# Kernel optimization log

Hardware: AMD Instinct MI355X
Metric: run time of the kernel (lower is better)

## Reference

```python
import jax, jax.numpy as jnp
from jax import lax
import numpy as np

P = 9          # patch_size (hardcoded in CUTSEncoder)
HALF = P // 2  # 4
EPS = 1e-5     # BatchNorm eps (torch default)
SLOPE = 0.01   # LeakyReLU negative slope (torch default)


def _conv(x, w, b):
    # 3x3 'same' conv, NCHW / OIHW
    y = lax.conv_general_dilated(x, w, (1, 1), 'SAME',
                                 dimension_numbers=('NCHW', 'OIHW', 'NCHW'))
    return y + b[None, :, None, None]


def _bn(x, gamma, beta):
    # training-mode BatchNorm2d: batch statistics over (N,H,W)
    m = jnp.mean(x, axis=(0, 2, 3), keepdims=True)
    v = jnp.var(x, axis=(0, 2, 3), keepdims=True)
    return gamma[None, :, None, None] * (x - m) * lax.rsqrt(v + EPS) + beta[None, :, None, None]


def _block(x, w, b, g, be):
    return jax.nn.leaky_relu(_bn(_conv(x, w, b), g, be), SLOPE)


def setup_inputs() -> dict:
    key = jax.random.key(0)
    ks = jax.random.split(key, 16)
    B, C, H, W = 8, 3, 256, 256
    K = 32                 # num_kernels
    L = K * 8              # latent_dim = 256
    S = 32                 # sampled_patches_per_image

    x = jax.random.normal(ks[0], (B, C, H, W), jnp.float32)
    anchors_hw = jax.random.randint(ks[1], (B, S, 2), HALF, H - HALF, jnp.int32)
    positives_hw = jax.random.randint(ks[2], (B, S, 2), HALF, H - HALF, jnp.int32)

    def w_(k, shape):
        return jax.random.normal(k, shape, jnp.float32) * 0.05

    params = {
        'w1': w_(ks[3], (K, C, 3, 3)),       'b1': jnp.zeros((K,), jnp.float32),
        'g1': jnp.ones((K,), jnp.float32),   'be1': jnp.zeros((K,), jnp.float32),
        'w2': w_(ks[4], (2 * K, K, 3, 3)),   'b2': jnp.zeros((2 * K,), jnp.float32),
        'g2': jnp.ones((2 * K,), jnp.float32), 'be2': jnp.zeros((2 * K,), jnp.float32),
        'w3': w_(ks[5], (4 * K, 2 * K, 3, 3)), 'b3': jnp.zeros((4 * K,), jnp.float32),
        'g3': jnp.ones((4 * K,), jnp.float32), 'be3': jnp.zeros((4 * K,), jnp.float32),
        'w4': w_(ks[6], (8 * K, 4 * K, 3, 3)), 'b4': jnp.zeros((8 * K,), jnp.float32),
        'g4': jnp.ones((8 * K,), jnp.float32), 'be4': jnp.zeros((8 * K,), jnp.float32),
        'rw': w_(ks[7], (S * C * P * P, S * L)),  # recon Linear [out,in]
        'rb': jnp.zeros((S * C * P * P,), jnp.float32),
    }
    return dict(x=x, anchors_hw=anchors_hw, positives_hw=positives_hw, **params)


def reference(x, anchors_hw, positives_hw,
              w1, b1, g1, be1, w2, b2, g2, be2,
              w3, b3, g3, be3, w4, b4, g4, be4, rw, rb):
    B, C, H, W = x.shape
    # 4-stage conv+BN+LeakyReLU backbone -> z: [B, L, H, W]
    z = _block(x, w1, b1, g1, be1)
    z = _block(z, w2, b2, g2, be2)
    z = _block(z, w3, b3, g3, be3)
    z = _block(z, w4, b4, g4, be4)

    # batched 9x9 patch extraction around anchors: [B, S, C, P, P]
    def patch(img, hw):  # img: [C,H,W], hw: [2]
        return lax.dynamic_slice(img, (0, hw[0] - HALF, hw[1] - HALF), (C, P, P))
    x_anchors = jax.vmap(lambda img, hws: jax.vmap(lambda hw: patch(img, hw))(hws))(x, anchors_hw)

    # batched pointwise latent gathers: [B, S, L]
    def gather_z(zb, hws):  # zb: [L,H,W]
        return zb[:, hws[:, 0], hws[:, 1]].T  # [S, L]
    z_anchors = jax.vmap(gather_z)(z, anchors_hw)
    z_positives = jax.vmap(gather_z)(z, positives_hw)

    x_anchors_flat = x_anchors.reshape(B, -1)
    x_recon = z_anchors.reshape(B, -1) @ rw.T + rb
    return (z, x_anchors_flat, x_recon, z_anchors, z_positives)
```

## Files before the change

### kernel.cpp

```cpp
#include <hip/hip_runtime.h>
#include <hip/hip_bf16.h>

#define HW 65536
constexpr int IMG_W = 256;

typedef __attribute__((ext_vector_type(8))) short short8;
typedef __attribute__((ext_vector_type(4))) float f32x4;

__device__ __forceinline__ float bf2f(unsigned short u) {
    return __uint_as_float(((unsigned)u) << 16);
}
__device__ __forceinline__ unsigned short f2bf(float f) {
    __hip_bfloat16 h = __float2bfloat16(f);
    return *reinterpret_cast<unsigned short*>(&h);
}

__global__ __launch_bounds__(256) void conv1_direct(
    const float* __restrict__ x, const float* __restrict__ wt,
    const float* __restrict__ bias, unsigned short* __restrict__ outraw)
{
    constexpr int CIN = 3, COUT = 32, OCB = 16;
    const int tile = blockIdx.x;
    const int ty0 = (tile >> 3) << 5;
    const int tx0 = (tile & 7) << 5;
    const int oc0 = blockIdx.y * OCB;
    const int b = blockIdx.z;

    __shared__ alignas(16) float s_in[CIN][34][36];
    __shared__ alignas(16) float s_w[CIN][9][OCB];

    const int tid = threadIdx.x;
    const int lx = tid & 31;
    const int ly = tid >> 5;

    float acc[4][OCB];
    #pragma unroll
    for (int j = 0; j < 4; ++j)
        #pragma unroll
        for (int oc = 0; oc < OCB; ++oc) acc[j][oc] = 0.f;

    for (int idx = tid; idx < CIN * 34 * 34; idx += 256) {
        int ic  = idx / (34 * 34);
        int rem = idx - ic * (34 * 34);
        int r   = rem / 34;
        int cc  = rem - r * 34;
        int gy = ty0 - 1 + r, gx = tx0 - 1 + cc;
        float v = 0.f;
        if ((unsigned)gy < 256u && (unsigned)gx < 256u)
            v = x[((size_t)(b * CIN + ic)) * HW + (size_t)gy * IMG_W + gx];
        s_in[ic][r][cc] = v;
    }
    for (int idx = tid; idx < CIN * 9 * OCB; idx += 256) {
        int oc  = idx & (OCB - 1);
        int t2  = idx >> 4;
        int tap = t2 % 9;
        int ic  = t2 / 9;
        s_w[ic][tap][oc] = wt[((size_t)(oc0 + oc) * CIN + ic) * 9 + tap];
    }
    __syncthreads();

    for (int ic = 0; ic < CIN; ++ic) {
        #pragma unroll
        for (int tap = 0; tap < 9; ++tap) {
            const int dy = tap / 3, dx = tap % 3;
            float wr[OCB];
            #pragma unroll
            for (int q = 0; q < OCB / 4; ++q)
                *(float4*)&wr[q * 4] = *(const float4*)&s_w[ic][tap][q * 4];
            #pragma unroll
            for (int j = 0; j < 4; ++j) {
                float iv = s_in[ic][ly + 8 * j + dy][lx + dx];
                #pragma unroll
                for (int oc = 0; oc < OCB; ++oc) acc[j][oc] += iv * wr[oc];
            }
        }
    }

    #pragma unroll
    for (int j = 0; j < 4; ++j) {
        const size_t p = ((size_t)b << 16) + (size_t)((ty0 + ly + 8 * j) << 8) + tx0 + lx;
        short8 v0, v1;
        #pragma unroll
        for (int k = 0; k < 8; ++k) {
            v0[k] = (short)f2bf(acc[j][k] + bias[oc0 + k]);
            v1[k] = (short)f2bf(acc[j][8 + k] + bias[oc0 + 8 + k]);
        }
        *(short8*)&outraw[p * COUT + oc0]     = v0;
        *(short8*)&outraw[p * COUT + oc0 + 8] = v1;
    }
}

__global__ void repack2(const float* __restrict__ w, unsigned short* __restrict__ wp,
                        int COUT, int CIN)
{
    int i = blockIdx.x * 256 + threadIdx.x;
    int K9 = 9 * CIN;
    if (i >= COUT * K9) return;
    int oc = i / K9, k = i - oc * K9;
    int tap = k / CIN, ic = k - tap * CIN;
    wp[(size_t)(k >> 3) * COUT * 8 + oc * 8 + (k & 7)] =
        f2bf(w[((size_t)(oc * CIN + ic)) * 9 + tap]);
}

template<int CIN, int COUT, int WM, int WN>
__global__ __launch_bounds__(256, 3) void conv_mfma2(
    const unsigned short* __restrict__ in, const float2* __restrict__ coef,
    const unsigned short* __restrict__ wp, const float* __restrict__ bias,
    unsigned short* __restrict__ outraw, float2* __restrict__ partial)
{
    constexpr int CINP = CIN + 8;
    constexpr int ROWS = WM * 4;
    constexpr int TILES = (256 / ROWS) * 16;
    constexpr int NOC = COUT / (WN * 64);
    constexpr int NCHUNK = TILES * 8;
    constexpr int ICB = CIN / 32;
    constexpr int NOCT = CIN / 8;

    __shared__ alignas(16) short s_in[(ROWS + 2) * 18 * CINP];
    __shared__ float2 s_coef[CIN];
    __shared__ float2 s_stat[4][64];

    const int bx = blockIdx.x;
    const int tile = bx / NOC;
    const int oc0 = (bx - tile * NOC) * (WN * 64);
    const int b = blockIdx.z;
    const int ty0 = (tile >> 4) * ROWS;
    const int tx0 = (tile & 15) * 16;
    const int tid = threadIdx.x;

    if (tid < CIN) s_coef[tid] = coef[tid];
    __syncthreads();

    const size_t bbase = (size_t)b << 16;
    for (int idx = tid; idx < (ROWS + 2) * 18 * NOCT; idx += 256) {
        int ic8 = idx % NOCT;
        int rc  = idx / NOCT;
        int c = rc % 18, r = rc / 18;
        int gy = ty0 - 1 + r, gx = tx0 - 1 + c;
        short8 v = (short8)0;
        if ((unsigned)gy < 256u && (unsigned)gx < 256u) {
            short8 rawv = *(const short8*)&in[(bbase + (size_t)(gy << 8) + gx) * CIN + ic8 * 8];
            #pragma unroll
            for (int j = 0; j < 8; ++j) {
                float2 ab = s_coef[ic8 * 8 + j];
                float xv = ab.x * bf2f((unsigned short)rawv[j]) + ab.y;
                xv = xv > 0.f ? xv : 0.01f * xv;
                v[j] = (short)f2bf(xv);
            }
        }
        *(short8*)&s_in[(r * 18 + c) * CINP + ic8 * 8] = v;
    }
    __syncthreads();

    const int lane = tid & 63;
    const int wv = tid >> 6;
    const int wm = wv / WN, wn = wv % WN;
    const int ln = lane & 15;
    const int grp = lane >> 4;

    f32x4 acc[4][4] = {};

    const unsigned short* wpb = wp + ((size_t)grp * COUT + oc0 + wn * 64 + ln) * 8;

    for (int tap = 0; tap < 9; ++tap) {
        const int dy = tap / 3, dx = tap - dy * 3;
        const int arow = (wm * 4 + dy) * 18 + ln + dx;
        const int kc0 = tap * (CIN / 8);
        #pragma unroll
        for (int icb = 0; icb < ICB; ++icb) {
            short8 bfr[4];
            #pragma unroll
            for (int g = 0; g < 4; ++g)
                bfr[g] = *(const short8*)&wpb[((size_t)(kc0 + icb * 4) * COUT + g * 16) * 8];
            #pragma unroll
            for (int f = 0; f < 4; ++f) {
                short8 av = *(const short8*)&s_in[(arow + f * 18) * CINP + icb * 32 + grp * 8];
                #pragma unroll
                for (int g = 0; g < 4; ++g)
                    acc[f][g] = __builtin_amdgcn_mfma_f32_16x16x32_bf16(av, bfr[g], acc[f][g], 0, 0, 0);
            }
        }
    }

    #pragma unroll
    for (int g = 0; g < 4; ++g) {
        const int oc = oc0 + wn * 64 + g * 16 + ln;
        const float bv = bias[oc];
        float s = 0.f, q = 0.f;
        #pragma unroll
        for (int f = 0; f < 4; ++f) {
            const int rr = ty0 + wm * 4 + f;
            const size_t rowbase = (bbase + (size_t)(rr << 8) + tx0 + grp * 4) * COUT + oc;
            #pragma unroll
            for (int reg = 0; reg < 4; ++reg) {
                float v = acc[f][g][reg] + bv;
                outraw[rowbase + (size_t)reg * COUT] = f2bf(v);
                s += v; q += v * v;
            }
        }
        s += __shfl_down(s, 32); q += __shfl_down(q, 32);
        s += __shfl_down(s, 16); q += __shfl_down(q, 16);
        if (grp == 0) s_stat[wv][g * 16 + ln] = make_float2(s, q);
    }
    __syncthreads();
    if (tid < WN * 64) {
        const int wn2 = tid >> 6;
        const int ol = tid & 63;
        float sx = 0.f, sq = 0.f;
        #pragma unroll
        for (int m = 0; m < WM; ++m) {
            float2 p = s_stat[m * WN + wn2][ol];
            sx += p.x; sq += p.y;
        }
        const int chunk = b * TILES + tile;
        partial[(size_t)(oc0 + wn2 * 64 + ol) * NCHUNK + chunk] = make_float2(sx, sq);
    }
}

template<int C>
__global__ __launch_bounds__(256) void bn_stats_nhwc(const unsigned short* __restrict__ raw,
                                                     float2* __restrict__ partial)
{
    constexpr int CPT = C / 8;
    constexpr int PPI = 256 / CPT;
    const int t = threadIdx.x;
    const int co = t % CPT, pg = t / CPT;
    const int p0 = blockIdx.x * 2048;
    float s[8], ss[8];
    #pragma unroll
    for (int j = 0; j < 8; ++j) { s[j] = 0.f; ss[j] = 0.f; }
    for (int p = p0 + pg; p < p0 + 2048; p += PPI) {
        short8 v = *(const short8*)&raw[(size_t)p * C + co * 8];
        #pragma unroll
        for (int j = 0; j < 8; ++j) {
            float xv = bf2f((unsigned short)v[j]);
            s[j] += xv; ss[j] += xv * xv;
        }
    }
    __shared__ float rs[256][8], rss[256][8];
    #pragma unroll
    for (int j = 0; j < 8; ++j) { rs[t][j] = s[j]; rss[t][j] = ss[j]; }
    __syncthreads();
    for (int off = PPI / 2; off > 0; off >>= 1) {
        if (pg < off) {
            #pragma unroll
            for (int j = 0; j < 8; ++j) {
                rs[t][j]  += rs[t + off * CPT][j];
                rss[t][j] += rss[t + off * CPT][j];
            }
        }
        __syncthreads();
    }
    if (pg == 0) {
        #pragma unroll
        for (int j = 0; j < 8; ++j)
            partial[(size_t)(co * 8 + j) * 256 + blockIdx.x] = make_float2(rs[t][j], rss[t][j]);
    }
}

__global__ void bn_finalize_kernel(const float2* __restrict__ partial,
                                   const float* __restrict__ gamma,
                                   const float* __restrict__ beta,
                                   float2* __restrict__ coef, int C, int nchunk)
{
    int c = threadIdx.x;
    if (c >= C) return;
    float s = 0.f, ss = 0.f;
    for (int i = 0; i < nchunk; ++i) {
        float2 p = partial[(size_t)c * nchunk + i];
        s += p.x; ss += p.y;
    }
    const float N = 524288.f;
    float m = s / N;
    float v = ss / N - m * m;
    float rsq = rsqrtf(v + 1e-5f);
    float a = gamma[c] * rsq;
    coef[c] = make_float2(a, beta[c] - m * a);
}

template<int NCHUNK>
__global__ __launch_bounds__(256) void bn_finalize2(const float2* __restrict__ partial,
                                                    const float* __restrict__ gamma,
                                                    const float* __restrict__ beta,
                                                    float2* __restrict__ coef)
{
    const int c = blockIdx.x, t = threadIdx.x;
    float s = 0.f, q = 0.f;
    for (int i = t; i < NCHUNK; i += 256) {
        float2 p = partial[(size_t)c * NCHUNK + i];
        s += p.x; q += p.y;
    }
    __shared__ float rs[256], rq[256];
    rs[t] = s; rq[t] = q;
    __syncthreads();
    for (int off = 128; off; off >>= 1) {
        if (t < off) { rs[t] += rs[t + off]; rq[t] += rq[t + off]; }
        __syncthreads();
    }
    if (t == 0) {
        const float N = 524288.f;
        float m = rs[0] / N;
        float v = rq[0] / N - m * m;
        float a = gamma[c] * rsqrtf(v + 1e-5f);
        coef[c] = make_float2(a, beta[c] - m * a);
    }
}

__global__ __launch_bounds__(256) void apply_t(const unsigned short* __restrict__ raw,
                                               const float2* __restrict__ coef,
                                               float* __restrict__ z)
{
    __shared__ float s_t[256 * 36];
    __shared__ float2 s_c[256];
    const int t = threadIdx.x;
    s_c[t] = coef[t];
    __syncthreads();

    const size_t p0 = (size_t)blockIdx.x * 32;
    const int o = t & 31, prow = t >> 5;
    #pragma unroll
    for (int it = 0; it < 4; ++it) {
        const int pxi = prow + it * 8;
        short8 v = *(const short8*)&raw[(p0 + pxi) * 256 + o * 8];
        #pragma unroll
        for (int j = 0; j < 8; ++j) {
            const int oc = o * 8 + j;
            float2 ab = s_c[oc];
            float xv = ab.x * bf2f((unsigned short)v[j]) + ab.y;
            xv = xv > 0.f ? xv : 0.01f * xv;
            s_t[oc * 36 + (pxi ^ ((o & 7) * 4))] = xv;
        }
    }
    __syncthreads();

    const int Q = t & 7, ocr = t >> 3;
    const int b = (int)(p0 >> 16);
    const int pxl = (int)(p0 & 65535);
    #pragma unroll
    for (int pass = 0; pass < 8; ++pass) {
        const int oc = ocr + pass * 32;
        const int w = (oc >> 3) & 7;
        f32x4 vv = *(const f32x4*)&s_t[oc * 36 + ((Q ^ w) * 4)];
        *(f32x4*)&z[(((size_t)(b * 256 + oc)) << 16) + pxl + Q * 4] = vv;
    }
}

__global__ void patches_kernel(const float* __restrict__ x, const int* __restrict__ hw,
                               float* __restrict__ out)
{
    int bs = blockIdx.x;
    int b = bs >> 5;
    int h = hw[bs * 2], w = hw[bs * 2 + 1];
    int t = threadIdx.x;
    if (t < 243) {
        int c = t / 81, r = (t / 9) % 9, cc = t % 9;
        out[(size_t)bs * 243 + t] =
            x[((size_t)(b * 3 + c)) * HW + (size_t)(h - 4 + r) * IMG_W + (w - 4 + cc)];
    }
}

__global__ void gather_kernel(const float* __restrict__ z, const int* __restrict__ hw,
                              float* __restrict__ out)
{
    int bs = blockIdx.x;
    int b = bs >> 5;
    int h = hw[bs * 2], w = hw[bs * 2 + 1];
    int l = threadIdx.x;
    out[(size_t)bs * 256 + l] = z[((size_t)(b * 256 + l)) * HW + (size_t)h * IMG_W + w];
}

__global__ __launch_bounds__(256) void recon_kernel(const float* __restrict__ za,
                                                    const float* __restrict__ rw,
                                                    const float* __restrict__ rb,
                                                    float* __restrict__ out)
{
    int wave = threadIdx.x >> 6, lane = threadIdx.x & 63;
    int n0 = blockIdx.x * 16 + wave * 4;
    float acc[4][8];
    #pragma unroll
    for (int j = 0; j < 4; ++j)
        #pragma unroll
        for (int bb = 0; bb < 8; ++bb) acc[j][bb] = 0.f;

    for (int i = 0; i < 32; ++i) {
        int k = i * 256 + lane * 4;
        float4 wv[4];
        #pragma unroll
        for (int j = 0; j < 4; ++j)
            wv[j] = *(const float4*)&rw[(size_t)(n0 + j) * 8192 + k];
        #pragma unroll
        for (int bb = 0; bb < 8; ++bb) {
            float4 zv = *(const float4*)&za[(size_t)bb * 8192 + k];
            #pragma unroll
            for (int j = 0; j < 4; ++j)
                acc[j][bb] += zv.x * wv[j].x + zv.y * wv[j].y + zv.z * wv[j].z + zv.w * wv[j].w;
        }
    }
    #pragma unroll
    for (int j = 0; j < 4; ++j)
        #pragma unroll
        for (int bb = 0; bb < 8; ++bb) {
            float v = acc[j][bb];
            #pragma unroll
            for (int off = 32; off; off >>= 1) v += __shfl_down(v, off);
            if (lane == 0) out[(size_t)bb * 7776 + n0 + j] = v + rb[n0 + j];
        }
}

extern "C" void kernel_launch(void* const* d_in, const int* in_sizes, int n_in,
                              void* d_out, int out_size, void* d_ws, size_t ws_size,
                              hipStream_t stream) {
    (void)in_sizes; (void)n_in; (void)out_size; (void)ws_size;

    const float* x        = (const float*)d_in[0];
    const int* anchors    = (const int*)d_in[1];
    const int* positives  = (const int*)d_in[2];
    const float* w1 = (const float*)d_in[3];  const float* b1 = (const float*)d_in[4];
    const float* g1 = (const float*)d_in[5];  const float* be1 = (const float*)d_in[6];
    const float* w2 = (const float*)d_in[7];  const float* b2 = (const float*)d_in[8];
    const float* g2 = (const float*)d_in[9];  const float* be2 = (const float*)d_in[10];
    const float* w3 = (const float*)d_in[11]; const float* b3 = (const float*)d_in[12];
    const float* g3 = (const float*)d_in[13]; const float* be3 = (const float*)d_in[14];
    const float* w4 = (const float*)d_in[15]; const float* b4 = (const float*)d_in[16];
    const float* g4 = (const float*)d_in[17]; const float* be4 = (const float*)d_in[18];
    const float* rw = (const float*)d_in[19]; const float* rb = (const float*)d_in[20];

    float* z  = (float*)d_out;
    float* xa = z + 134217728;
    float* xr = xa + 62208;
    float* za = xr + 62208;
    float* zp = za + 65536;

    char* zb = (char*)d_out;
    unsigned short* raw1 = (unsigned short*)zb;
    unsigned short* raw2 = (unsigned short*)(zb + 33554432ull);
    unsigned short* raw3 = (unsigned short*)(zb + 100663296ull);

    char* ws = (char*)d_ws;
    unsigned short* wp   = (unsigned short*)ws;
    float2* partial = (float2*)(ws + 1048576ull);
    float2* coef1   = (float2*)(ws + 10485760ull);
    float2* coef2   = coef1 + 256;
    float2* coef3   = coef2 + 256;
    float2* coef4   = coef3 + 256;
    unsigned short* raw4 = (unsigned short*)(ws + 16777216ull);

    conv1_direct<<<dim3(64, 2, 8), 256, 0, stream>>>(x, w1, b1, raw1);
    bn_stats_nhwc<32><<<256, 256, 0, stream>>>(raw1, partial);
    bn_finalize_kernel<<<1, 256, 0, stream>>>(partial, g1, be1, coef1, 32, 256);

    repack2<<<(64 * 288 + 255) / 256, 256, 0, stream>>>(w2, wp, 64, 32);
    conv_mfma2<32, 64, 4, 1><<<dim3(256, 1, 8), 256, 0, stream>>>(raw1, coef1, wp, b2, raw2, partial);
    bn_finalize2<2048><<<64, 256, 0, stream>>>(partial, g2, be2, coef2);

    repack2<<<(128 * 576 + 255) / 256, 256, 0, stream>>>(w3, wp, 128, 64);
    conv_mfma2<64, 128, 2, 2><<<dim3(512, 1, 8), 256, 0, stream>>>(raw2, coef2, wp, b3, raw3, partial);
    bn_finalize2<4096><<<128, 256, 0, stream>>>(partial, g3, be3, coef3);

    repack2<<<(256 * 1152 + 255) / 256, 256, 0, stream>>>(w4, wp, 256, 128);
    conv_mfma2<128, 256, 2, 2><<<dim3(1024, 1, 8), 256, 0, stream>>>(raw3, coef3, wp, b4, raw4, partial);
    bn_finalize2<4096><<<256, 256, 0, stream>>>(partial, g4, be4, coef4);

    apply_t<<<16384, 256, 0, stream>>>(raw4, coef4, z);

    patches_kernel<<<256, 256, 0, stream>>>(x, anchors, xa);
    gather_kernel<<<256, 256, 0, stream>>>(z, anchors, za);
    gather_kernel<<<256, 256, 0, stream>>>(z, positives, zp);
    recon_kernel<<<486, 256, 0, stream>>>(za, rw, rb, xr);
}
```

Measured before the change: 809.5 us.

## Cover full output channels per block and swap MFMA operands for vector stores

```diff
diff --git a/kernel.cpp b/kernel.cpp
--- a/kernel.cpp
+++ b/kernel.cpp
@@ -102,27 +102,26 @@
         f2bf(w[((size_t)(oc * CIN + ic)) * 9 + tap]);
 }
 
-template<int CIN, int COUT, int WM, int WN>
-__global__ __launch_bounds__(256, 3) void conv_mfma2(
+template<int CIN, int COUT, int WM, int WN, int WOC>
+__global__ __launch_bounds__(256, 2) void conv_mfma3(
     const unsigned short* __restrict__ in, const float2* __restrict__ coef,
     const unsigned short* __restrict__ wp, const float* __restrict__ bias,
     unsigned short* __restrict__ outraw, float2* __restrict__ partial)
 {
+    static_assert(WN * WOC == COUT, "block must cover full COUT");
     constexpr int CINP = CIN + 8;
     constexpr int ROWS = WM * 4;
+    constexpr int NOCT = CIN / 8;
+    constexpr int NG = WOC / 16;
+    constexpr int ICB = CIN / 32;
     constexpr int TILES = (256 / ROWS) * 16;
-    constexpr int NOC = COUT / (WN * 64);
     constexpr int NCHUNK = TILES * 8;
-    constexpr int ICB = CIN / 32;
-    constexpr int NOCT = CIN / 8;
 
     __shared__ alignas(16) short s_in[(ROWS + 2) * 18 * CINP];
     __shared__ float2 s_coef[CIN];
-    __shared__ float2 s_stat[4][64];
-
-    const int bx = blockIdx.x;
-    const int tile = bx / NOC;
-    const int oc0 = (bx - tile * NOC) * (WN * 64);
+    __shared__ float2 s_stat[4][128];
+
+    const int tile = blockIdx.x;
     const int b = blockIdx.z;
     const int ty0 = (tile >> 4) * ROWS;
     const int tx0 = (tile & 15) * 16;
@@ -143,8 +142,8 @@
             #pragma unroll
             for (int j = 0; j < 8; ++j) {
                 float2 ab = s_coef[ic8 * 8 + j];
-                float xv = ab.x * bf2f((unsigned short)rawv[j]) + ab.y;
-                xv = xv > 0.f ? xv : 0.01f * xv;
+                float xv = fmaf(ab.x, bf2f((unsigned short)rawv[j]), ab.y);
+                xv = fmaxf(xv, 0.01f * xv);
                 v[j] = (short)f2bf(xv);
             }
         }
@@ -158,9 +157,9 @@
     const int ln = lane & 15;
     const int grp = lane >> 4;
 
-    f32x4 acc[4][4] = {};
-
-    const unsigned short* wpb = wp + ((size_t)grp * COUT + oc0 + wn * 64 + ln) * 8;
+    f32x4 acc[4][NG] = {};
+
+    const unsigned short* wpb = wp + ((size_t)grp * COUT + wn * WOC + ln) * 8;
 
     for (int tap = 0; tap < 9; ++tap) {
         const int dy = tap / 3, dx = tap - dy * 3;
@@ -168,52 +167,59 @@
         const int kc0 = tap * (CIN / 8);
         #pragma unroll
         for (int icb = 0; icb < ICB; ++icb) {
-            short8 bfr[4];
-            #pragma unroll
-            for (int g = 0; g < 4; ++g)
-                bfr[g] = *(const short8*)&wpb[((size_t)(kc0 + icb * 4) * COUT + g * 16) * 8];
+            short8 wfr[NG];
+            #pragma unroll
+            for (int g = 0; g < NG; ++g)
+                wfr[g] = *(const short8*)&wpb[((size_t)(kc0 + icb * 4) * COUT + g * 16) * 8];
             #pragma unroll
             for (int f = 0; f < 4; ++f) {
-                short8 av = *(const short8*)&s_in[(arow + f * 18) * CINP + icb * 32 + grp * 8];
+                short8 px = *(const short8*)&s_in[(arow + f * 18) * CINP + icb * 32 + grp * 8];
                 #pragma unroll
-                for (int g = 0; g < 4; ++g)
-                    acc[f][g] = __builtin_amdgcn_mfma_f32_16x16x32_bf16(av, bfr[g], acc[f][g], 0, 0, 0);
+                for (int g = 0; g < NG; ++g)
+                    acc[f][g] = __builtin_amdgcn_mfma_f32_16x16x32_bf16(wfr[g], px, acc[f][g], 0, 0, 0);
             }
         }
     }
 
     #pragma unroll
-    for (int g = 0; g < 4; ++g) {
-        const int oc = oc0 + wn * 64 + g * 16 + ln;
-        const float bv = bias[oc];
-        float s = 0.f, q = 0.f;
+    for (int g = 0; g < NG; ++g) {
+        const int ocl = wn * WOC + g * 16 + grp * 4;
+        const f32x4 bias4 = *(const f32x4*)&bias[ocl];
+        f32x4 vs = {}, vq = {};
         #pragma unroll
         for (int f = 0; f < 4; ++f) {
-            const int rr = ty0 + wm * 4 + f;
-            const size_t rowbase = (bbase + (size_t)(rr << 8) + tx0 + grp * 4) * COUT + oc;
-            #pragma unroll
-            for (int reg = 0; reg < 4; ++reg) {
-                float v = acc[f][g][reg] + bv;
-                outraw[rowbase + (size_t)reg * COUT] = f2bf(v);
-                s += v; q += v * v;
+            const int row = ty0 + wm * 4 + f;
+            f32x4 v = acc[f][g] + bias4;
+            vs += v; vq += v * v;
+            short4 sv;
+            sv.x = (short)f2bf(v[0]); sv.y = (short)f2bf(v[1]);
+            sv.z = (short)f2bf(v[2]); sv.w = (short)f2bf(v[3]);
+            *(short4*)&outraw[(bbase + (size_t)(row << 8) + tx0 + ln) * COUT + ocl] = sv;
+        }
+        #pragma unroll
+        for (int d = 1; d < 16; d <<= 1) {
+            #pragma unroll
+            for (int r = 0; r < 4; ++r) {
+                vs[r] += __shfl_xor(vs[r], d);
+                vq[r] += __shfl_xor(vq[r], d);
             }
         }
-        s += __shfl_down(s, 32); q += __shfl_down(q, 32);
-        s += __shfl_down(s, 16); q += __shfl_down(q, 16);
-        if (grp == 0) s_stat[wv][g * 16 + ln] = make_float2(s, q);
-    }
-    __syncthreads();
-    if (tid < WN * 64) {
-        const int wn2 = tid >> 6;
-        const int ol = tid & 63;
+        if (ln == 0) {
+            #pragma unroll
+            for (int r = 0; r < 4; ++r)
+                s_stat[wv][g * 16 + grp * 4 + r] = make_float2(vs[r], vq[r]);
+        }
+    }
+    __syncthreads();
+    if (tid < COUT) {
+        const int wn_o = tid / WOC, ol = tid - wn_o * WOC;
         float sx = 0.f, sq = 0.f;
         #pragma unroll
         for (int m = 0; m < WM; ++m) {
-            float2 p = s_stat[m * WN + wn2][ol];
+            float2 p = s_stat[m * WN + wn_o][ol];
             sx += p.x; sq += p.y;
         }
-        const int chunk = b * TILES + tile;
-        partial[(size_t)(oc0 + wn2 * 64 + ol) * NCHUNK + chunk] = make_float2(sx, sq);
+        partial[(size_t)tid * NCHUNK + b * TILES + tile] = make_float2(sx, sq);
     }
 }
 
@@ -326,8 +332,8 @@
         for (int j = 0; j < 8; ++j) {
             const int oc = o * 8 + j;
             float2 ab = s_c[oc];
-            float xv = ab.x * bf2f((unsigned short)v[j]) + ab.y;
-            xv = xv > 0.f ? xv : 0.01f * xv;
+            float xv = fmaf(ab.x, bf2f((unsigned short)v[j]), ab.y);
+            xv = fmaxf(xv, 0.01f * xv);
             s_t[oc * 36 + (pxi ^ ((o & 7) * 4))] = xv;
         }
     }
@@ -450,15 +456,15 @@
     bn_finalize_kernel<<<1, 256, 0, stream>>>(partial, g1, be1, coef1, 32, 256);
 
     repack2<<<(64 * 288 + 255) / 256, 256, 0, stream>>>(w2, wp, 64, 32);
-    conv_mfma2<32, 64, 4, 1><<<dim3(256, 1, 8), 256, 0, stream>>>(raw1, coef1, wp, b2, raw2, partial);
+    conv_mfma3<32, 64, 4, 1, 64><<<dim3(256, 1, 8), 256, 0, stream>>>(raw1, coef1, wp, b2, raw2, partial);
     bn_finalize2<2048><<<64, 256, 0, stream>>>(partial, g2, be2, coef2);
 
     repack2<<<(128 * 576 + 255) / 256, 256, 0, stream>>>(w3, wp, 128, 64);
-    conv_mfma2<64, 128, 2, 2><<<dim3(512, 1, 8), 256, 0, stream>>>(raw2, coef2, wp, b3, raw3, partial);
-    bn_finalize2<4096><<<128, 256, 0, stream>>>(partial, g3, be3, coef3);
+    conv_mfma3<64, 128, 4, 1, 128><<<dim3(256, 1, 8), 256, 0, stream>>>(raw2, coef2, wp, b3, raw3, partial);
+    bn_finalize2<2048><<<128, 256, 0, stream>>>(partial, g3, be3, coef3);
 
     repack2<<<(256 * 1152 + 255) / 256, 256, 0, stream>>>(w4, wp, 256, 128);
-    conv_mfma2<128, 256, 2, 2><<<dim3(1024, 1, 8), 256, 0, stream>>>(raw3, coef3, wp, b4, raw4, partial);
+    conv_mfma3<128, 256, 2, 2, 128><<<dim3(512, 1, 8), 256, 0, stream>>>(raw3, coef3, wp, b4, raw4, partial);
     bn_finalize2<4096><<<256, 256, 0, stream>>>(partial, g4, be4, coef4);
 
     apply_t<<<16384, 256, 0, stream>>>(raw4, coef4, z);
```

New measurement: 828.9 us. 2.4% more time.
